# Performance work log

Measured on AMD Instinct MI355X. Metric: run time of the kernel, lower is better.

Reference implementation:

```python
import jax, jax.numpy as jnp
import numpy as np

B, S, E, H, HD, RD, MP = 2, 2048, 1024, 16, 64, 32, 8  # batch, seq, embed, heads, head_dim, rotary_dim, mp_num


def rotate_every_two(x):
    # x: [..., D] -> interleave (-x_odd, x_even)
    x1 = x[..., ::2]
    x2 = x[..., 1::2]
    return jnp.stack((-x2, x1), axis=-1).reshape(x.shape)


def apply_rotary(x, sin, cos):
    # x: [B,S,H,RD]; sin/cos: [S, RD//2] -> repeat_interleave(2) -> [1,S,1,RD]
    sin = jnp.repeat(sin, 2, axis=-1)[None, :, None, :]
    cos = jnp.repeat(cos, 2, axis=-1)[None, :, None, :]
    return x * cos + rotate_every_two(x) * sin


def setup_inputs() -> dict:
    key = jax.random.key(0)
    k1, k2, k3 = jax.random.split(key, 3)
    return {
        "hidden_states": jax.random.normal(k1, (B, S, E), dtype=jnp.float32),
        "w_qkv": jax.random.normal(k2, (3 * E, E), dtype=jnp.float32) * 0.02,
        "w_out": jax.random.normal(k3, (E, E), dtype=jnp.float32) * 0.02,
    }


def reference(hidden_states, w_qkv, w_out):
    qkv = hidden_states @ w_qkv.T                      # [B,S,3E]
    local = HD * H // MP                               # 128
    qkv = qkv.reshape(B, S, MP, 3 * local)
    # torch.split order in source is (query, value, key)
    q, v, k = jnp.split(qkv, 3, axis=-1)               # each [B,S,MP,local]

    def split_heads(x):
        return x.reshape(B, S, MP, H // MP, HD).reshape(B, S, H, HD)

    q, k, v = split_heads(q), split_heads(k), split_heads(v)  # [B,S,H,HD]

    # fixed sinusoidal rotary embedding over first RD dims
    inv_freq = 1.0 / 10000 ** (jnp.arange(0, RD, 2, dtype=jnp.float32) / RD)
    sinusoid = jnp.arange(S, dtype=jnp.float32)[:, None] * inv_freq[None, :]  # [S, RD//2]
    sin, cos = jnp.sin(sinusoid), jnp.cos(sinusoid)

    q = jnp.concatenate([apply_rotary(q[..., :RD], sin, cos), q[..., RD:]], axis=-1)
    k = jnp.concatenate([apply_rotary(k[..., :RD], sin, cos), k[..., RD:]], axis=-1)

    # [B,H,S,HD]
    q = q.transpose(0, 2, 1, 3)
    k = k.transpose(0, 2, 1, 3)
    v = v.transpose(0, 2, 1, 3)

    scores = jnp.einsum('bhqd,bhkd->bhqk', q, k) / np.float32(np.sqrt(HD))
    causal = jnp.tril(jnp.ones((S, S), dtype=bool))
    scores = jnp.where(causal[None, None], scores, jnp.float32(-1e9))
    attn = jax.nn.softmax(scores.astype(jnp.float32), axis=-1).astype(q.dtype)
    out = jnp.einsum('bhqk,bhkd->bhqd', attn, v)       # [B,H,S,HD]
    out = out.transpose(0, 2, 1, 3).reshape(B, S, E)
    return out @ w_out.T
```

## Files before the change

kernel.cpp:

```cpp
#include <hip/hip_runtime.h>

typedef __attribute__((ext_vector_type(8))) short short8;
typedef __attribute__((ext_vector_type(4))) float v4f;

#define ASYNC_COPY16(ldsptr, gptr)                                                        \
  __builtin_amdgcn_global_load_lds((const __attribute__((address_space(1))) void*)(gptr), \
                                   (__attribute__((address_space(3))) void*)(ldsptr),     \
                                   16, 0, 0)

__device__ __forceinline__ unsigned short f2bf(float f) {
  unsigned int u = __float_as_uint(f);
  u += 0x7fffu + ((u >> 16) & 1u);
  return (unsigned short)(u >> 16);
}
__device__ __forceinline__ float bf2f(unsigned short s) {
  return __uint_as_float(((unsigned int)s) << 16);
}

__global__ void convert_all(const float* __restrict__ h, const float* __restrict__ wq,
                            const float* __restrict__ wo, unsigned short* __restrict__ ho,
                            unsigned short* __restrict__ wqo, unsigned short* __restrict__ woo) {
  int i = (blockIdx.x * blockDim.x + threadIdx.x) * 4;
  const float* src;
  unsigned short* dst;
  int j;
  if (i < 4194304) { src = h; dst = ho; j = i; }
  else if (i < 7340032) { src = wq; dst = wqo; j = i - 4194304; }
  else { src = wo; dst = woo; j = i - 7340032; }
  float4 v = *(const float4*)(src + j);
  ushort4 o;
  o.x = f2bf(v.x); o.y = f2bf(v.y); o.z = f2bf(v.z); o.w = f2bf(v.w);
  *(ushort4*)(dst + j) = o;
}

template <int BN, bool BF16OUT>
__global__ __launch_bounds__(256) void gemm_bt(const unsigned short* __restrict__ A,
                                               const unsigned short* __restrict__ Bm,
                                               void* __restrict__ Cv, int M, int N, int K) {
  constexpr int WN = BN / 2;
  constexpr int JN = WN / 16;
  __shared__ __attribute__((aligned(16))) unsigned short As[128 * 32];
  __shared__ __attribute__((aligned(16))) unsigned short Bs[BN * 32];
  int t = threadIdx.x;
  int w = t >> 6, lane = t & 63, kb = lane >> 4, lr = lane & 15;
  int m0 = blockIdx.y * 128, n0 = blockIdx.x * BN;
  int wm = (w >> 1) * 64, wn = (w & 1) * WN;
  v4f acc[4][JN];
#pragma unroll
  for (int i = 0; i < 4; i++)
#pragma unroll
    for (int j = 0; j < JN; j++) acc[i][j] = (v4f){0.f, 0.f, 0.f, 0.f};
  int ra = m0 + (t >> 2);
  int rb = n0 + (t >> 2);
  int ca = (t & 3) * 8;
  for (int k0 = 0; k0 < K; k0 += 32) {
    ASYNC_COPY16(&As[t * 8],        A + (size_t)ra * K + k0 + ca);
    ASYNC_COPY16(&As[2048 + t * 8], A + (size_t)(ra + 64) * K + k0 + ca);
#pragma unroll
    for (int c = 0; c < BN / 64; c++)
      ASYNC_COPY16(&Bs[c * 2048 + t * 8], Bm + (size_t)(rb + c * 64) * K + k0 + ca);
    __syncthreads();
    short8 av[4], bv[JN];
#pragma unroll
    for (int i = 0; i < 4; i++) av[i] = *(const short8*)&As[(wm + i * 16 + lr) * 32 + kb * 8];
#pragma unroll
    for (int j = 0; j < JN; j++) bv[j] = *(const short8*)&Bs[(wn + j * 16 + lr) * 32 + kb * 8];
#pragma unroll
    for (int i = 0; i < 4; i++)
#pragma unroll
      for (int j = 0; j < JN; j++)
        acc[i][j] = __builtin_amdgcn_mfma_f32_16x16x32_bf16(av[i], bv[j], acc[i][j], 0, 0, 0);
    __syncthreads();
  }
#pragma unroll
  for (int i = 0; i < 4; i++) {
    int row = m0 + wm + i * 16 + kb * 4;
#pragma unroll
    for (int j = 0; j < JN; j++) {
      int col = n0 + wn + j * 16 + lr;
#pragma unroll
      for (int r = 0; r < 4; r++) {
        if (BF16OUT)
          ((unsigned short*)Cv)[(size_t)(row + r) * N + col] = f2bf(acc[i][j][r]);
        else
          ((float*)Cv)[(size_t)(row + r) * N + col] = acc[i][j][r];
      }
    }
  }
}

__global__ __launch_bounds__(256) void rope_vt(const unsigned short* __restrict__ qkv,
                                               unsigned short* __restrict__ Q,
                                               unsigned short* __restrict__ Ko,
                                               unsigned short* __restrict__ Vt) {
  __shared__ float tile[64][65];
  int t = threadIdx.x;
  int bh = blockIdx.y, s0 = blockIdx.x * 64;
  int b = bh >> 4, h = bh & 15;
  int mp = h >> 1, ii = h & 1;
  int hbase = mp * 384 + ii * 64;
  int tx = t & 63, ty = t >> 6;
#pragma unroll
  for (int q16 = 0; q16 < 16; q16++) {
    int srow = q16 * 4 + ty;
    tile[srow][tx] = bf2f(qkv[(size_t)(b * 2048 + s0 + srow) * 3072 + hbase + 128 + tx]);
  }
  int sl = t >> 2, ch = t & 3;
  int s = s0 + sl;
  size_t ib = (size_t)(b * 2048 + s) * 3072 + hbase + ch * 16;
  short8 qv0 = *(const short8*)(qkv + ib);
  short8 qv1 = *(const short8*)(qkv + ib + 8);
  short8 kv0 = *(const short8*)(qkv + ib + 256);
  short8 kv1 = *(const short8*)(qkv + ib + 264);
  float qf[16], kf[16];
#pragma unroll
  for (int j = 0; j < 8; j++) {
    qf[j] = bf2f((unsigned short)qv0[j]); qf[8 + j] = bf2f((unsigned short)qv1[j]);
    kf[j] = bf2f((unsigned short)kv0[j]); kf[8 + j] = bf2f((unsigned short)kv1[j]);
  }
  if (ch < 2) {
#pragma unroll
    for (int jj = 0; jj < 8; jj++) {
      int j = ch * 8 + jj;
      float ang = (float)s * expf(-(float)j * 0.57564627324851142f);
      float sn, cs;
      sincosf(ang, &sn, &cs);
      float a = qf[2 * jj], bq = qf[2 * jj + 1];
      qf[2 * jj] = a * cs - bq * sn; qf[2 * jj + 1] = bq * cs + a * sn;
      float c2 = kf[2 * jj], d2 = kf[2 * jj + 1];
      kf[2 * jj] = c2 * cs - d2 * sn; kf[2 * jj + 1] = d2 * cs + c2 * sn;
    }
  }
  const float qs = 0.125f * 1.4426950408889634f;
  unsigned short qo[16], ko[16];
#pragma unroll
  for (int j = 0; j < 16; j++) { qo[j] = f2bf(qs * qf[j]); ko[j] = f2bf(kf[j]); }
  size_t ob = (size_t)(bh * 2048 + s) * 64 + ch * 16;
  *(short8*)(Q + ob) = *(short8*)qo;
  *(short8*)(Q + ob + 8) = *(short8*)(qo + 8);
  *(short8*)(Ko + ob) = *(short8*)ko;
  *(short8*)(Ko + ob + 8) = *(short8*)(ko + 8);
  __syncthreads();
#pragma unroll
  for (int q16 = 0; q16 < 16; q16++) {
    int drow = q16 * 4 + ty;
    Vt[(size_t)bh * 64 * 2048 + (size_t)drow * 2048 + s0 + tx] = f2bf(tile[tx][drow]);
  }
}

__global__ __launch_bounds__(256) void attn_fused(const unsigned short* __restrict__ Qg,
                                                  const unsigned short* __restrict__ Kg,
                                                  const unsigned short* __restrict__ Vtg,
                                                  unsigned short* __restrict__ AO) {
  __shared__ __attribute__((aligned(16))) unsigned short Ks[2 * 64 * 64];
  __shared__ __attribute__((aligned(16))) unsigned short Vs[2 * 64 * 64];
  __shared__ __attribute__((aligned(16))) unsigned short Ps[4 * 16 * 64];
  int t = threadIdx.x;
  int w = t >> 6, lane = t & 63, kb = lane >> 4, lr = lane & 15;
  int gid = blockIdx.x;
  int bh = gid >> 5;
  int qtile = ((gid & 31) + bh) & 31;
  int m0 = qtile * 64;
  const unsigned short* Qb = Qg + (size_t)bh * 2048 * 64;
  const unsigned short* Kb = Kg + (size_t)bh * 2048 * 64;
  const unsigned short* Vb = Vtg + (size_t)bh * 64 * 2048;

  short8 aq0 = *(const short8*)(Qb + (size_t)(m0 + w * 16 + lr) * 64 + kb * 8);
  short8 aq1 = *(const short8*)(Qb + (size_t)(m0 + w * 16 + lr) * 64 + 32 + kb * 8);

  v4f acc[4];
  float lp[4];
#pragma unroll
  for (int n = 0; n < 4; n++) acc[n] = (v4f){0.f, 0.f, 0.f, 0.f};
#pragma unroll
  for (int r = 0; r < 4; r++) lp[r] = 0.f;

  int nkt = qtile + 1;

  auto stage = [&](int kt, int buf) {
    int base = buf * 4096;
#pragma unroll
    for (int rep = 0; rep < 2; rep++) {
      int slot = rep * 256 + t;
      int row = slot >> 3;
      int gc = (slot & 7) ^ (row & 7);
      ASYNC_COPY16(&Ks[base + slot * 8], Kb + (size_t)(kt * 64 + row) * 64 + gc * 8);
      ASYNC_COPY16(&Vs[base + slot * 8], Vb + (size_t)row * 2048 + kt * 64 + gc * 8);
    }
  };

  stage(0, 0);
  __syncthreads();

  int sw = lr & 7;
  unsigned short* Pw = &Ps[w * 16 * 64];
  for (int kt = 0; kt < nkt; kt++) {
    int cur = (kt & 1) * 4096;
    if (kt + 1 < nkt) stage(kt + 1, (kt + 1) & 1);
    v4f sc[4];
#pragma unroll
    for (int n2 = 0; n2 < 4; n2++) {
      int row = n2 * 16 + lr;
      short8 bk0 = *(const short8*)&Ks[cur + row * 64 + (kb ^ sw) * 8];
      short8 bk1 = *(const short8*)&Ks[cur + row * 64 + ((kb + 4) ^ sw) * 8];
      v4f z = (v4f){0.f, 0.f, 0.f, 0.f};
      z = __builtin_amdgcn_mfma_f32_16x16x32_bf16(aq0, bk0, z, 0, 0, 0);
      z = __builtin_amdgcn_mfma_f32_16x16x32_bf16(aq1, bk1, z, 0, 0, 0);
      sc[n2] = z;
    }
    if (kt == nkt - 1) {
#pragma unroll
      for (int n2 = 0; n2 < 4; n2++)
#pragma unroll
        for (int r = 0; r < 4; r++)
          if (n2 * 16 + lr > w * 16 + kb * 4 + r) sc[n2][r] = -1e30f;
    }
#pragma unroll
    for (int n2 = 0; n2 < 4; n2++)
#pragma unroll
      for (int r = 0; r < 4; r++) {
        float p = exp2f(sc[n2][r]);
        lp[r] += p;
        int rp = kb * 4 + r;
        Pw[rp * 64 + ((n2 * 2 + (lr >> 3)) ^ (rp & 7)) * 8 + (lr & 7)] = f2bf(p);
      }
    short8 ap0 = *(const short8*)&Pw[lr * 64 + (kb ^ sw) * 8];
    short8 ap1 = *(const short8*)&Pw[lr * 64 + ((kb + 4) ^ sw) * 8];
#pragma unroll
    for (int n = 0; n < 4; n++) {
      int d = n * 16 + lr;
      short8 bv0 = *(const short8*)&Vs[cur + d * 64 + (kb ^ sw) * 8];
      short8 bv1 = *(const short8*)&Vs[cur + d * 64 + ((kb + 4) ^ sw) * 8];
      acc[n] = __builtin_amdgcn_mfma_f32_16x16x32_bf16(ap0, bv0, acc[n], 0, 0, 0);
      acc[n] = __builtin_amdgcn_mfma_f32_16x16x32_bf16(ap1, bv1, acc[n], 0, 0, 0);
    }
    __syncthreads();
  }
#pragma unroll
  for (int r = 0; r < 4; r++) {
#pragma unroll
    for (int off = 1; off < 16; off <<= 1) lp[r] += __shfl_xor(lp[r], off);
    lp[r] = 1.0f / lp[r];
  }
  int b = bh >> 4, h = bh & 15;
#pragma unroll
  for (int n = 0; n < 4; n++)
#pragma unroll
    for (int r = 0; r < 4; r++) {
      int qrow = m0 + w * 16 + kb * 4 + r;
      AO[(size_t)(b * 2048 + qrow) * 1024 + h * 64 + n * 16 + lr] = f2bf(acc[n][r] * lp[r]);
    }
}

extern "C" void kernel_launch(void* const* d_in, const int* in_sizes, int n_in,
                              void* d_out, int out_size, void* d_ws, size_t ws_size,
                              hipStream_t stream) {
  const float* hidden = (const float*)d_in[0];
  const float* w_qkv = (const float*)d_in[1];
  const float* w_out = (const float*)d_in[2];
  float* out = (float*)d_out;
  char* ws = (char*)d_ws;
  unsigned short* hid_bf = (unsigned short*)(ws);
  unsigned short* wqkv_bf = (unsigned short*)(ws + (8ull << 20));
  unsigned short* wout_bf = (unsigned short*)(ws + (14ull << 20));
  unsigned short* qkv_bf = (unsigned short*)(ws + (16ull << 20));
  unsigned short* Qb = (unsigned short*)(ws + (40ull << 20));
  unsigned short* Kb = (unsigned short*)(ws + (48ull << 20));
  unsigned short* Vt = (unsigned short*)(ws + (56ull << 20));
  unsigned short* AO = (unsigned short*)(ws + (64ull << 20));

  convert_all<<<8192, 256, 0, stream>>>(hidden, w_qkv, w_out, hid_bf, wqkv_bf, wout_bf);
  gemm_bt<128, true><<<dim3(24, 32), 256, 0, stream>>>(hid_bf, wqkv_bf, qkv_bf, 4096, 3072, 1024);
  rope_vt<<<dim3(32, 32), 256, 0, stream>>>(qkv_bf, Qb, Kb, Vt);
  attn_fused<<<1024, 256, 0, stream>>>(Qb, Kb, Vt, AO);
  gemm_bt<64, false><<<dim3(16, 32), 256, 0, stream>>>(AO, wout_bf, out, 4096, 1024, 1024);
}
```

Measured before the change: 214.0 us.

## Restructure attention into 128-key tiles with paired causal q-tiles and split-K waves

The attention kernel now gives each block two query tiles (pr and 31-pr) so every block does the same amount of causal work, and it launches half as many blocks. Each step loads 128-key K/V tiles. The four waves are arranged 2x2, with each wave covering 32 query rows and one 64-key half. The two key halves' partial outputs and row sums are combined through LDS before normalisation. This is meant to raise MFMA reuse per LDS load, cut loop iterations and balance the causal triangle, at the cost of an extra LDS reduction, more registers, and wasted masked work on diagonal tiles.

```diff
diff --git a/kernel.cpp b/kernel.cpp
--- a/kernel.cpp
+++ b/kernel.cpp
@@ -152,104 +152,151 @@
                                                   const unsigned short* __restrict__ Kg,
                                                   const unsigned short* __restrict__ Vtg,
                                                   unsigned short* __restrict__ AO) {
-  __shared__ __attribute__((aligned(16))) unsigned short Ks[2 * 64 * 64];
-  __shared__ __attribute__((aligned(16))) unsigned short Vs[2 * 64 * 64];
-  __shared__ __attribute__((aligned(16))) unsigned short Ps[4 * 16 * 64];
+  __shared__ __attribute__((aligned(16))) unsigned short Ks[2 * 128 * 64];
+  __shared__ __attribute__((aligned(16))) unsigned short Vs[2 * 64 * 128];
+  __shared__ __attribute__((aligned(16))) unsigned short Ps[4 * 32 * 64];
   int t = threadIdx.x;
   int w = t >> 6, lane = t & 63, kb = lane >> 4, lr = lane & 15;
+  int wq = w >> 1, wk = w & 1;
   int gid = blockIdx.x;
-  int bh = gid >> 5;
-  int qtile = ((gid & 31) + bh) & 31;
-  int m0 = qtile * 64;
+  int bh = gid >> 4, pr = gid & 15;
   const unsigned short* Qb = Qg + (size_t)bh * 2048 * 64;
   const unsigned short* Kb = Kg + (size_t)bh * 2048 * 64;
   const unsigned short* Vb = Vtg + (size_t)bh * 64 * 2048;
-
-  short8 aq0 = *(const short8*)(Qb + (size_t)(m0 + w * 16 + lr) * 64 + kb * 8);
-  short8 aq1 = *(const short8*)(Qb + (size_t)(m0 + w * 16 + lr) * 64 + 32 + kb * 8);
-
-  v4f acc[4];
-  float lp[4];
-#pragma unroll
-  for (int n = 0; n < 4; n++) acc[n] = (v4f){0.f, 0.f, 0.f, 0.f};
-#pragma unroll
-  for (int r = 0; r < 4; r++) lp[r] = 0.f;
-
-  int nkt = qtile + 1;
+  int b = bh >> 4, h = bh & 15;
+  int sw = lr & 7;
+  unsigned short* Pw = &Ps[w * 32 * 64];
+  float* accS = (float*)Ps;
+  float* lpS = (float*)Ks;
 
   auto stage = [&](int kt, int buf) {
-    int base = buf * 4096;
-#pragma unroll
-    for (int rep = 0; rep < 2; rep++) {
-      int slot = rep * 256 + t;
-      int row = slot >> 3;
-      int gc = (slot & 7) ^ (row & 7);
-      ASYNC_COPY16(&Ks[base + slot * 8], Kb + (size_t)(kt * 64 + row) * 64 + gc * 8);
-      ASYNC_COPY16(&Vs[base + slot * 8], Vb + (size_t)row * 2048 + kt * 64 + gc * 8);
+    int base = buf * 8192;
+#pragma unroll
+    for (int rep = 0; rep < 4; rep++) {
+      int s = rep * 256 + t;
+      int krow = s >> 3;
+      int kgc = (s & 7) ^ (krow & 7);
+      ASYNC_COPY16(&Ks[base + s * 8], Kb + (size_t)(kt * 128 + krow) * 64 + kgc * 8);
+      int vrow = s >> 4;
+      int vgc = (s & 15) ^ (vrow & 7);
+      ASYNC_COPY16(&Vs[base + s * 8], Vb + (size_t)vrow * 2048 + kt * 128 + vgc * 8);
     }
   };
 
-  stage(0, 0);
-  __syncthreads();
-
-  int sw = lr & 7;
-  unsigned short* Pw = &Ps[w * 16 * 64];
-  for (int kt = 0; kt < nkt; kt++) {
-    int cur = (kt & 1) * 4096;
-    if (kt + 1 < nkt) stage(kt + 1, (kt + 1) & 1);
-    v4f sc[4];
-#pragma unroll
-    for (int n2 = 0; n2 < 4; n2++) {
-      int row = n2 * 16 + lr;
-      short8 bk0 = *(const short8*)&Ks[cur + row * 64 + (kb ^ sw) * 8];
-      short8 bk1 = *(const short8*)&Ks[cur + row * 64 + ((kb + 4) ^ sw) * 8];
-      v4f z = (v4f){0.f, 0.f, 0.f, 0.f};
-      z = __builtin_amdgcn_mfma_f32_16x16x32_bf16(aq0, bk0, z, 0, 0, 0);
-      z = __builtin_amdgcn_mfma_f32_16x16x32_bf16(aq1, bk1, z, 0, 0, 0);
-      sc[n2] = z;
-    }
-    if (kt == nkt - 1) {
-#pragma unroll
-      for (int n2 = 0; n2 < 4; n2++)
-#pragma unroll
-        for (int r = 0; r < 4; r++)
-          if (n2 * 16 + lr > w * 16 + kb * 4 + r) sc[n2][r] = -1e30f;
-    }
-#pragma unroll
-    for (int n2 = 0; n2 < 4; n2++)
-#pragma unroll
-      for (int r = 0; r < 4; r++) {
-        float p = exp2f(sc[n2][r]);
-        lp[r] += p;
-        int rp = kb * 4 + r;
-        Pw[rp * 64 + ((n2 * 2 + (lr >> 3)) ^ (rp & 7)) * 8 + (lr & 7)] = f2bf(p);
-      }
-    short8 ap0 = *(const short8*)&Pw[lr * 64 + (kb ^ sw) * 8];
-    short8 ap1 = *(const short8*)&Pw[lr * 64 + ((kb + 4) ^ sw) * 8];
-#pragma unroll
-    for (int n = 0; n < 4; n++) {
-      int d = n * 16 + lr;
-      short8 bv0 = *(const short8*)&Vs[cur + d * 64 + (kb ^ sw) * 8];
-      short8 bv1 = *(const short8*)&Vs[cur + d * 64 + ((kb + 4) ^ sw) * 8];
-      acc[n] = __builtin_amdgcn_mfma_f32_16x16x32_bf16(ap0, bv0, acc[n], 0, 0, 0);
-      acc[n] = __builtin_amdgcn_mfma_f32_16x16x32_bf16(ap1, bv1, acc[n], 0, 0, 0);
-    }
-    __syncthreads();
-  }
-#pragma unroll
-  for (int r = 0; r < 4; r++) {
-#pragma unroll
-    for (int off = 1; off < 16; off <<= 1) lp[r] += __shfl_xor(lp[r], off);
-    lp[r] = 1.0f / lp[r];
-  }
-  int b = bh >> 4, h = bh & 15;
-#pragma unroll
-  for (int n = 0; n < 4; n++)
-#pragma unroll
-    for (int r = 0; r < 4; r++) {
-      int qrow = m0 + w * 16 + kb * 4 + r;
-      AO[(size_t)(b * 2048 + qrow) * 1024 + h * 64 + n * 16 + lr] = f2bf(acc[n][r] * lp[r]);
-    }
+  for (int half = 0; half < 2; half++) {
+    int qtile = half ? (31 - pr) : pr;
+    int m0 = qtile * 64;
+    int nkt = (qtile >> 1) + 1;
+    short8 aq[2][2];
+#pragma unroll
+    for (int m = 0; m < 2; m++) {
+      int row = m0 + wq * 32 + m * 16 + lr;
+#pragma unroll
+      for (int c = 0; c < 2; c++)
+        aq[m][c] = *(const short8*)(Qb + (size_t)row * 64 + c * 32 + kb * 8);
+    }
+    v4f acc[2][4];
+    v4f lp[2];
+#pragma unroll
+    for (int m = 0; m < 2; m++) {
+      lp[m] = (v4f){0.f, 0.f, 0.f, 0.f};
+#pragma unroll
+      for (int dt = 0; dt < 4; dt++) acc[m][dt] = (v4f){0.f, 0.f, 0.f, 0.f};
+    }
+    stage(0, 0);
+    __syncthreads();
+    for (int kt = 0; kt < nkt; kt++) {
+      int cur = (kt & 1) * 8192;
+      if (kt + 1 < nkt) stage(kt + 1, (kt + 1) & 1);
+      v4f sc[2][4];
+#pragma unroll
+      for (int n = 0; n < 4; n++) {
+        int krow = wk * 64 + n * 16 + lr;
+        short8 bk0 = *(const short8*)&Ks[cur + krow * 64 + ((kb) ^ sw) * 8];
+        short8 bk1 = *(const short8*)&Ks[cur + krow * 64 + ((kb + 4) ^ sw) * 8];
+#pragma unroll
+        for (int m = 0; m < 2; m++) {
+          v4f z = (v4f){0.f, 0.f, 0.f, 0.f};
+          z = __builtin_amdgcn_mfma_f32_16x16x32_bf16(aq[m][0], bk0, z, 0, 0, 0);
+          z = __builtin_amdgcn_mfma_f32_16x16x32_bf16(aq[m][1], bk1, z, 0, 0, 0);
+          sc[m][n] = z;
+        }
+      }
+      if (kt == nkt - 1) {
+#pragma unroll
+        for (int m = 0; m < 2; m++)
+#pragma unroll
+          for (int n = 0; n < 4; n++)
+#pragma unroll
+            for (int r = 0; r < 4; r++) {
+              int keya = kt * 128 + wk * 64 + n * 16 + lr;
+              int qrow = m0 + wq * 32 + m * 16 + kb * 4 + r;
+              if (keya > qrow) sc[m][n][r] = -1e30f;
+            }
+      }
+#pragma unroll
+      for (int m = 0; m < 2; m++)
+#pragma unroll
+        for (int n = 0; n < 4; n++)
+#pragma unroll
+          for (int r = 0; r < 4; r++) {
+            float p = exp2f(sc[m][n][r]);
+            lp[m][r] += p;
+            int rp = m * 16 + kb * 4 + r;
+            Pw[rp * 64 + ((n * 2 + (lr >> 3)) ^ (rp & 7)) * 8 + (lr & 7)] = f2bf(p);
+          }
+#pragma unroll
+      for (int ks = 0; ks < 2; ks++) {
+        short8 ap[2];
+#pragma unroll
+        for (int m = 0; m < 2; m++)
+          ap[m] = *(const short8*)&Pw[(m * 16 + lr) * 64 + ((ks * 4 + kb) ^ sw) * 8];
+#pragma unroll
+        for (int dt = 0; dt < 4; dt++) {
+          int d = dt * 16 + lr;
+          short8 bv = *(const short8*)&Vs[cur + d * 128 + ((wk * 8 + ks * 4 + kb) ^ sw) * 8];
+#pragma unroll
+          for (int m = 0; m < 2; m++)
+            acc[m][dt] = __builtin_amdgcn_mfma_f32_16x16x32_bf16(ap[m], bv, acc[m][dt], 0, 0, 0);
+        }
+      }
+      __syncthreads();
+    }
+    if (wk == 1) {
+#pragma unroll
+      for (int m = 0; m < 2; m++) {
+#pragma unroll
+        for (int dt = 0; dt < 4; dt++)
+          *(v4f*)&accS[wq * 2048 + (m * 4 + dt) * 256 + lane * 4] = acc[m][dt];
+        *(v4f*)&lpS[wq * 512 + lane * 8 + m * 4] = lp[m];
+      }
+    }
+    __syncthreads();
+    if (wk == 0) {
+#pragma unroll
+      for (int m = 0; m < 2; m++) {
+#pragma unroll
+        for (int dt = 0; dt < 4; dt++)
+          acc[m][dt] += *(v4f*)&accS[wq * 2048 + (m * 4 + dt) * 256 + lane * 4];
+        lp[m] += *(v4f*)&lpS[wq * 512 + lane * 8 + m * 4];
+      }
+#pragma unroll
+      for (int m = 0; m < 2; m++)
+#pragma unroll
+        for (int r = 0; r < 4; r++) {
+          float s = lp[m][r];
+#pragma unroll
+          for (int off = 1; off < 16; off <<= 1) s += __shfl_xor(s, off);
+          float inv = 1.0f / s;
+          int qrow = m0 + wq * 32 + m * 16 + kb * 4 + r;
+#pragma unroll
+          for (int dt = 0; dt < 4; dt++)
+            AO[(size_t)(b * 2048 + qrow) * 1024 + h * 64 + dt * 16 + lr] =
+                f2bf(acc[m][dt][r] * inv);
+        }
+    }
+    __syncthreads();
+  }
 }
 
 extern "C" void kernel_launch(void* const* d_in, const int* in_sizes, int n_in,
@@ -272,6 +319,6 @@
   convert_all<<<8192, 256, 0, stream>>>(hidden, w_qkv, w_out, hid_bf, wqkv_bf, wout_bf);
   gemm_bt<128, true><<<dim3(24, 32), 256, 0, stream>>>(hid_bf, wqkv_bf, qkv_bf, 4096, 3072, 1024);
   rope_vt<<<dim3(32, 32), 256, 0, stream>>>(qkv_bf, Qb, Kb, Vt);
-  attn_fused<<<1024, 256, 0, stream>>>(Qb, Kb, Vt, AO);
+  attn_fused<<<512, 256, 0, stream>>>(Qb, Kb, Vt, AO);
   gemm_bt<64, false><<<dim3(16, 32), 256, 0, stream>>>(AO, wout_bf, out, 4096, 1024, 1024);
 }
```

Result: slower. 226.9 us (+6.0%).

## Halve attention key tile to 32 with permuted V layout and smaller LDS

Applied to the files above, without the earlier changes.

The fused attention kernel now processes keys in tiles of 32 instead of 64. LDS for K, V and P drops to half or less and the launch bounds request 6 blocks per CU for higher occupancy. V is written with a permuted column order so the P fragment packs as bf16 pairs and one MFMA per dt covers the 32-key slice. The XOR swizzles are replaced by a column-chunk-major LDS layout. The price is twice as many loop iterations and barriers per block, with a finer causal-mask boundary across two tiles.

```diff
diff --git a/kernel.cpp b/kernel.cpp
--- a/kernel.cpp
+++ b/kernel.cpp
@@ -1,4 +1,5 @@
 #include <hip/hip_runtime.h>
+#include <hip/hip_bf16.h>
 
 typedef __attribute__((ext_vector_type(8))) short short8;
 typedef __attribute__((ext_vector_type(4))) float v4f;
@@ -144,17 +145,18 @@
 #pragma unroll
   for (int q16 = 0; q16 < 16; q16++) {
     int drow = q16 * 4 + ty;
-    Vt[(size_t)bh * 64 * 2048 + (size_t)drow * 2048 + s0 + tx] = f2bf(tile[tx][drow]);
-  }
-}
-
-__global__ __launch_bounds__(256) void attn_fused(const unsigned short* __restrict__ Qg,
-                                                  const unsigned short* __restrict__ Kg,
-                                                  const unsigned short* __restrict__ Vtg,
-                                                  unsigned short* __restrict__ AO) {
-  __shared__ __attribute__((aligned(16))) unsigned short Ks[2 * 64 * 64];
-  __shared__ __attribute__((aligned(16))) unsigned short Vs[2 * 64 * 64];
-  __shared__ __attribute__((aligned(16))) unsigned short Ps[4 * 16 * 64];
+    int p = ((tx & 15) * 2 + ((tx >> 4) & 1)) | (tx & 32);
+    Vt[(size_t)bh * 64 * 2048 + (size_t)drow * 2048 + s0 + p] = f2bf(tile[tx][drow]);
+  }
+}
+
+__global__ __launch_bounds__(256, 6) void attn_fused(const unsigned short* __restrict__ Qg,
+                                                     const unsigned short* __restrict__ Kg,
+                                                     const unsigned short* __restrict__ Vtg,
+                                                     unsigned short* __restrict__ AO) {
+  __shared__ __attribute__((aligned(16))) unsigned short Ks[2 * 2048];
+  __shared__ __attribute__((aligned(16))) unsigned short Vs[2 * 2048];
+  __shared__ __attribute__((aligned(16))) unsigned short Ps[4 * 16 * 40];
   int t = threadIdx.x;
   int w = t >> 6, lane = t & 63, kb = lane >> 4, lr = lane & 15;
   int gid = blockIdx.x;
@@ -175,81 +177,73 @@
 #pragma unroll
   for (int r = 0; r < 4; r++) lp[r] = 0.f;
 
-  int nkt = qtile + 1;
-
+  int nkt = 2 * qtile + 2;
+  int mrow = w * 16 + kb * 4;
+
+  int kc = t >> 5, krow_s = t & 31;
+  int vc = t >> 6, vd = t & 63;
   auto stage = [&](int kt, int buf) {
-    int base = buf * 4096;
-#pragma unroll
-    for (int rep = 0; rep < 2; rep++) {
-      int slot = rep * 256 + t;
-      int row = slot >> 3;
-      int gc = (slot & 7) ^ (row & 7);
-      ASYNC_COPY16(&Ks[base + slot * 8], Kb + (size_t)(kt * 64 + row) * 64 + gc * 8);
-      ASYNC_COPY16(&Vs[base + slot * 8], Vb + (size_t)row * 2048 + kt * 64 + gc * 8);
-    }
+    int base = buf * 2048;
+    ASYNC_COPY16(&Ks[base + t * 8], Kb + (size_t)(kt * 32 + krow_s) * 64 + kc * 8);
+    ASYNC_COPY16(&Vs[base + t * 8], Vb + (size_t)vd * 2048 + kt * 32 + vc * 8);
   };
 
   stage(0, 0);
   __syncthreads();
 
-  int sw = lr & 7;
-  unsigned short* Pw = &Ps[w * 16 * 64];
+  unsigned short* Pw = &Ps[w * 640];
   for (int kt = 0; kt < nkt; kt++) {
-    int cur = (kt & 1) * 4096;
+    int cur = (kt & 1) * 2048;
     if (kt + 1 < nkt) stage(kt + 1, (kt + 1) & 1);
-    v4f sc[4];
-#pragma unroll
-    for (int n2 = 0; n2 < 4; n2++) {
-      int row = n2 * 16 + lr;
-      short8 bk0 = *(const short8*)&Ks[cur + row * 64 + (kb ^ sw) * 8];
-      short8 bk1 = *(const short8*)&Ks[cur + row * 64 + ((kb + 4) ^ sw) * 8];
+    v4f sc[2];
+#pragma unroll
+    for (int n2 = 0; n2 < 2; n2++) {
+      int krow = n2 * 16 + lr;
+      short8 bk0 = *(const short8*)&Ks[cur + (kb * 32 + krow) * 8];
+      short8 bk1 = *(const short8*)&Ks[cur + ((kb + 4) * 32 + krow) * 8];
       v4f z = (v4f){0.f, 0.f, 0.f, 0.f};
       z = __builtin_amdgcn_mfma_f32_16x16x32_bf16(aq0, bk0, z, 0, 0, 0);
       z = __builtin_amdgcn_mfma_f32_16x16x32_bf16(aq1, bk1, z, 0, 0, 0);
       sc[n2] = z;
     }
-    if (kt == nkt - 1) {
-#pragma unroll
-      for (int n2 = 0; n2 < 4; n2++)
-#pragma unroll
-        for (int r = 0; r < 4; r++)
-          if (n2 * 16 + lr > w * 16 + kb * 4 + r) sc[n2][r] = -1e30f;
-    }
-#pragma unroll
-    for (int n2 = 0; n2 < 4; n2++)
-#pragma unroll
-      for (int r = 0; r < 4; r++) {
-        float p = exp2f(sc[n2][r]);
-        lp[r] += p;
-        int rp = kb * 4 + r;
-        Pw[rp * 64 + ((n2 * 2 + (lr >> 3)) ^ (rp & 7)) * 8 + (lr & 7)] = f2bf(p);
-      }
-    short8 ap0 = *(const short8*)&Pw[lr * 64 + (kb ^ sw) * 8];
-    short8 ap1 = *(const short8*)&Pw[lr * 64 + ((kb + 4) ^ sw) * 8];
-#pragma unroll
-    for (int n = 0; n < 4; n++) {
-      int d = n * 16 + lr;
-      short8 bv0 = *(const short8*)&Vs[cur + d * 64 + (kb ^ sw) * 8];
-      short8 bv1 = *(const short8*)&Vs[cur + d * 64 + ((kb + 4) ^ sw) * 8];
-      acc[n] = __builtin_amdgcn_mfma_f32_16x16x32_bf16(ap0, bv0, acc[n], 0, 0, 0);
-      acc[n] = __builtin_amdgcn_mfma_f32_16x16x32_bf16(ap1, bv1, acc[n], 0, 0, 0);
+    if (kt >= 2 * qtile) {
+#pragma unroll
+      for (int n2 = 0; n2 < 2; n2++)
+#pragma unroll
+        for (int r = 0; r < 4; r++) {
+          int key = kt * 32 + n2 * 16 + lr;
+          if (key > m0 + mrow + r) sc[n2][r] = -1e30f;
+        }
+    }
+#pragma unroll
+    for (int r = 0; r < 4; r++) {
+      float p0 = exp2f(sc[0][r]);
+      float p1 = exp2f(sc[1][r]);
+      lp[r] += p0 + p1;
+      __hip_bfloat162 pb = __float22bfloat162_rn(float2{p0, p1});
+      *(__hip_bfloat162*)&Pw[(mrow & 15) * 40 + r * 40 + lr * 2] = pb;
+    }
+    short8 ap = *(const short8*)&Pw[lr * 40 + kb * 8];
+#pragma unroll
+    for (int dt = 0; dt < 4; dt++) {
+      int d = dt * 16 + lr;
+      short8 bv = *(const short8*)&Vs[cur + (kb * 64 + d) * 8];
+      acc[dt] = __builtin_amdgcn_mfma_f32_16x16x32_bf16(ap, bv, acc[dt], 0, 0, 0);
     }
     __syncthreads();
   }
+  int b = bh >> 4, h = bh & 15;
 #pragma unroll
   for (int r = 0; r < 4; r++) {
-#pragma unroll
-    for (int off = 1; off < 16; off <<= 1) lp[r] += __shfl_xor(lp[r], off);
-    lp[r] = 1.0f / lp[r];
-  }
-  int b = bh >> 4, h = bh & 15;
-#pragma unroll
-  for (int n = 0; n < 4; n++)
-#pragma unroll
-    for (int r = 0; r < 4; r++) {
-      int qrow = m0 + w * 16 + kb * 4 + r;
-      AO[(size_t)(b * 2048 + qrow) * 1024 + h * 64 + n * 16 + lr] = f2bf(acc[n][r] * lp[r]);
-    }
+    float s = lp[r];
+#pragma unroll
+    for (int off = 1; off < 16; off <<= 1) s += __shfl_xor(s, off);
+    float inv = 1.0f / s;
+    int qrow = m0 + mrow + r;
+#pragma unroll
+    for (int dt = 0; dt < 4; dt++)
+      AO[(size_t)(b * 2048 + qrow) * 1024 + h * 64 + dt * 16 + lr] = f2bf(acc[dt][r] * inv);
+  }
 }
 
 extern "C" void kernel_launch(void* const* d_in, const int* in_sizes, int n_in,
```

Measured after the change: 209.6 us. -2.1%, faster.

## Rewrite attention with 32x32x16 MFMA and 128-row query tiles

Applied to the files above, without the earlier changes.

Reworks the fused causal attention kernel so each wave owns 32 query rows and uses 32x32x16 bf16 MFMA with the transposed product (K·Q^T, V^T·P^T), which halves the grid to 512 blocks of 128 query rows. The LDS staging layout drops the XOR swizzle in favour of a column-chunk-major layout, and P gets a padded per-row buffer. Row-sum reduction shrinks to one shuffle and outputs are written as 4-element vectors. The goal is fewer, larger MFMAs and more K/V reuse per staged tile, at the cost of more registers (launch_bounds 256,2), wasted masked work on diagonal tiles, and possible LDS bank conflicts without the swizzle.

```diff
diff --git a/kernel.cpp b/kernel.cpp
--- a/kernel.cpp
+++ b/kernel.cpp
@@ -1,7 +1,9 @@
 #include <hip/hip_runtime.h>
+#include <hip/hip_bf16.h>
 
 typedef __attribute__((ext_vector_type(8))) short short8;
 typedef __attribute__((ext_vector_type(4))) float v4f;
+typedef __attribute__((ext_vector_type(16))) float v16f;
 
 #define ASYNC_COPY16(ldsptr, gptr)                                                        \
   __builtin_amdgcn_global_load_lds((const __attribute__((address_space(1))) void*)(gptr), \
@@ -148,108 +150,115 @@
   }
 }
 
-__global__ __launch_bounds__(256) void attn_fused(const unsigned short* __restrict__ Qg,
-                                                  const unsigned short* __restrict__ Kg,
-                                                  const unsigned short* __restrict__ Vtg,
-                                                  unsigned short* __restrict__ AO) {
-  __shared__ __attribute__((aligned(16))) unsigned short Ks[2 * 64 * 64];
-  __shared__ __attribute__((aligned(16))) unsigned short Vs[2 * 64 * 64];
-  __shared__ __attribute__((aligned(16))) unsigned short Ps[4 * 16 * 64];
+__global__ __launch_bounds__(256, 2) void attn_fused(const unsigned short* __restrict__ Qg,
+                                                     const unsigned short* __restrict__ Kg,
+                                                     const unsigned short* __restrict__ Vtg,
+                                                     unsigned short* __restrict__ AO) {
+  __shared__ __attribute__((aligned(16))) unsigned short Ks[2 * 4096];
+  __shared__ __attribute__((aligned(16))) unsigned short Vs[2 * 4096];
+  __shared__ __attribute__((aligned(16))) unsigned short Ps[4 * 32 * 68];
   int t = threadIdx.x;
-  int w = t >> 6, lane = t & 63, kb = lane >> 4, lr = lane & 15;
+  int w = t >> 6, lane = t & 63, l31 = lane & 31, hh = lane >> 5;
   int gid = blockIdx.x;
-  int bh = gid >> 5;
-  int qtile = ((gid & 31) + bh) & 31;
-  int m0 = qtile * 64;
+  int bh = gid >> 4;
+  int qtile = ((gid & 15) + (gid >> 4) + ((gid >> 8) << 3)) & 15;
+  int m0 = qtile * 128;
   const unsigned short* Qb = Qg + (size_t)bh * 2048 * 64;
   const unsigned short* Kb = Kg + (size_t)bh * 2048 * 64;
   const unsigned short* Vb = Vtg + (size_t)bh * 64 * 2048;
 
-  short8 aq0 = *(const short8*)(Qb + (size_t)(m0 + w * 16 + lr) * 64 + kb * 8);
-  short8 aq1 = *(const short8*)(Qb + (size_t)(m0 + w * 16 + lr) * 64 + 32 + kb * 8);
-
-  v4f acc[4];
-  float lp[4];
-#pragma unroll
-  for (int n = 0; n < 4; n++) acc[n] = (v4f){0.f, 0.f, 0.f, 0.f};
-#pragma unroll
-  for (int r = 0; r < 4; r++) lp[r] = 0.f;
-
-  int nkt = qtile + 1;
+  int qrow = m0 + w * 32 + l31;
+  short8 qf[4];
+#pragma unroll
+  for (int kc = 0; kc < 4; kc++)
+    qf[kc] = *(const short8*)(Qb + (size_t)qrow * 64 + kc * 16 + hh * 8);
+
+  v16f acc0, acc1;
+#pragma unroll
+  for (int r = 0; r < 16; r++) { acc0[r] = 0.f; acc1[r] = 0.f; }
+  float lp = 0.f;
+
+  int nkt = 2 * qtile + 2;
 
   auto stage = [&](int kt, int buf) {
     int base = buf * 4096;
 #pragma unroll
     for (int rep = 0; rep < 2; rep++) {
-      int slot = rep * 256 + t;
-      int row = slot >> 3;
-      int gc = (slot & 7) ^ (row & 7);
-      ASYNC_COPY16(&Ks[base + slot * 8], Kb + (size_t)(kt * 64 + row) * 64 + gc * 8);
-      ASYNC_COPY16(&Vs[base + slot * 8], Vb + (size_t)row * 2048 + kt * 64 + gc * 8);
+      int s = rep * 256 + t;
+      int c = s >> 6, rr = s & 63;
+      ASYNC_COPY16(&Ks[base + s * 8], Kb + (size_t)(kt * 64 + rr) * 64 + c * 8);
+      ASYNC_COPY16(&Vs[base + s * 8], Vb + (size_t)rr * 2048 + kt * 64 + c * 8);
     }
   };
 
   stage(0, 0);
   __syncthreads();
 
-  int sw = lr & 7;
-  unsigned short* Pw = &Ps[w * 16 * 64];
+  unsigned short* Pq = &Ps[(w * 32 + l31) * 68];
   for (int kt = 0; kt < nkt; kt++) {
     int cur = (kt & 1) * 4096;
     if (kt + 1 < nkt) stage(kt + 1, (kt + 1) & 1);
-    v4f sc[4];
-#pragma unroll
-    for (int n2 = 0; n2 < 4; n2++) {
-      int row = n2 * 16 + lr;
-      short8 bk0 = *(const short8*)&Ks[cur + row * 64 + (kb ^ sw) * 8];
-      short8 bk1 = *(const short8*)&Ks[cur + row * 64 + ((kb + 4) ^ sw) * 8];
-      v4f z = (v4f){0.f, 0.f, 0.f, 0.f};
-      z = __builtin_amdgcn_mfma_f32_16x16x32_bf16(aq0, bk0, z, 0, 0, 0);
-      z = __builtin_amdgcn_mfma_f32_16x16x32_bf16(aq1, bk1, z, 0, 0, 0);
-      sc[n2] = z;
-    }
-    if (kt == nkt - 1) {
-#pragma unroll
-      for (int n2 = 0; n2 < 4; n2++)
-#pragma unroll
-        for (int r = 0; r < 4; r++)
-          if (n2 * 16 + lr > w * 16 + kb * 4 + r) sc[n2][r] = -1e30f;
-    }
-#pragma unroll
-    for (int n2 = 0; n2 < 4; n2++)
-#pragma unroll
-      for (int r = 0; r < 4; r++) {
-        float p = exp2f(sc[n2][r]);
-        lp[r] += p;
-        int rp = kb * 4 + r;
-        Pw[rp * 64 + ((n2 * 2 + (lr >> 3)) ^ (rp & 7)) * 8 + (lr & 7)] = f2bf(p);
+    v16f sc[2];
+#pragma unroll
+    for (int kg = 0; kg < 2; kg++) {
+      v16f z;
+#pragma unroll
+      for (int r = 0; r < 16; r++) z[r] = 0.f;
+#pragma unroll
+      for (int kc = 0; kc < 4; kc++) {
+        short8 kf = *(const short8*)&Ks[cur + ((2 * kc + hh) * 64 + kg * 32 + l31) * 8];
+        z = __builtin_amdgcn_mfma_f32_32x32x16_bf16(kf, qf[kc], z, 0, 0, 0);
       }
-    short8 ap0 = *(const short8*)&Pw[lr * 64 + (kb ^ sw) * 8];
-    short8 ap1 = *(const short8*)&Pw[lr * 64 + ((kb + 4) ^ sw) * 8];
-#pragma unroll
-    for (int n = 0; n < 4; n++) {
-      int d = n * 16 + lr;
-      short8 bv0 = *(const short8*)&Vs[cur + d * 64 + (kb ^ sw) * 8];
-      short8 bv1 = *(const short8*)&Vs[cur + d * 64 + ((kb + 4) ^ sw) * 8];
-      acc[n] = __builtin_amdgcn_mfma_f32_16x16x32_bf16(ap0, bv0, acc[n], 0, 0, 0);
-      acc[n] = __builtin_amdgcn_mfma_f32_16x16x32_bf16(ap1, bv1, acc[n], 0, 0, 0);
+      sc[kg] = z;
+    }
+    if (kt * 64 + 63 > m0 + w * 32) {
+#pragma unroll
+      for (int kg = 0; kg < 2; kg++)
+#pragma unroll
+        for (int r = 0; r < 16; r++) {
+          int key = kt * 64 + kg * 32 + (r & 3) + 8 * (r >> 2) + 4 * hh;
+          if (key > qrow) sc[kg][r] = -1e30f;
+        }
+    }
+#pragma unroll
+    for (int kg = 0; kg < 2; kg++)
+#pragma unroll
+      for (int qd = 0; qd < 4; qd++) {
+        unsigned short pk[4];
+#pragma unroll
+        for (int r = 0; r < 4; r++) {
+          float p = exp2f(sc[kg][qd * 4 + r]);
+          lp += p;
+          pk[r] = f2bf(p);
+        }
+        *(uint2*)&Pq[kg * 32 + qd * 8 + hh * 4] = *(uint2*)pk;
+      }
+#pragma unroll
+    for (int kc = 0; kc < 4; kc++) {
+      short8 pf = *(const short8*)&Pq[kc * 16 + hh * 8];
+      short8 vf0 = *(const short8*)&Vs[cur + ((2 * kc + hh) * 64 + l31) * 8];
+      short8 vf1 = *(const short8*)&Vs[cur + ((2 * kc + hh) * 64 + 32 + l31) * 8];
+      acc0 = __builtin_amdgcn_mfma_f32_32x32x16_bf16(vf0, pf, acc0, 0, 0, 0);
+      acc1 = __builtin_amdgcn_mfma_f32_32x32x16_bf16(vf1, pf, acc1, 0, 0, 0);
     }
     __syncthreads();
   }
-#pragma unroll
-  for (int r = 0; r < 4; r++) {
-#pragma unroll
-    for (int off = 1; off < 16; off <<= 1) lp[r] += __shfl_xor(lp[r], off);
-    lp[r] = 1.0f / lp[r];
-  }
+  lp += __shfl_xor(lp, 32);
+  float inv = 1.0f / lp;
   int b = bh >> 4, h = bh & 15;
-#pragma unroll
-  for (int n = 0; n < 4; n++)
+  size_t obase = (size_t)(b * 2048 + qrow) * 1024 + h * 64;
+#pragma unroll
+  for (int qd = 0; qd < 4; qd++) {
+    unsigned short o0[4], o1[4];
 #pragma unroll
     for (int r = 0; r < 4; r++) {
-      int qrow = m0 + w * 16 + kb * 4 + r;
-      AO[(size_t)(b * 2048 + qrow) * 1024 + h * 64 + n * 16 + lr] = f2bf(acc[n][r] * lp[r]);
-    }
+      o0[r] = f2bf(acc0[qd * 4 + r] * inv);
+      o1[r] = f2bf(acc1[qd * 4 + r] * inv);
+    }
+    int d0 = qd * 8 + hh * 4;
+    *(uint2*)&AO[obase + d0] = *(uint2*)o0;
+    *(uint2*)&AO[obase + 32 + d0] = *(uint2*)o1;
+  }
 }
 
 extern "C" void kernel_launch(void* const* d_in, const int* in_sizes, int n_in,
@@ -272,6 +281,6 @@
   convert_all<<<8192, 256, 0, stream>>>(hidden, w_qkv, w_out, hid_bf, wqkv_bf, wout_bf);
   gemm_bt<128, true><<<dim3(24, 32), 256, 0, stream>>>(hid_bf, wqkv_bf, qkv_bf, 4096, 3072, 1024);
   rope_vt<<<dim3(32, 32), 256, 0, stream>>>(qkv_bf, Qb, Kb, Vt);
-  attn_fused<<<1024, 256, 0, stream>>>(Qb, Kb, Vt, AO);
+  attn_fused<<<512, 256, 0, stream>>>(Qb, Kb, Vt, AO);
   gemm_bt<64, false><<<dim3(16, 32), 256, 0, stream>>>(AO, wout_bf, out, 4096, 1024, 1024);
 }
```

Result: slower. 220.3 us (+2.9%).
